# Optimization experiments

Measured on AMD Instinct MI355X. Metric: run time of the kernel, lower is better.

## Reference

```python
import jax, jax.numpy as jnp
import numpy as np

HIDDEN = 1024
RANK = 4
INPUT = 16
ALPHA = 0.1
BASE_SCALE = 500.0
B = 32
T = 1024


def setup_inputs() -> dict:
    key = jax.random.key(0)
    k1, k2, k3, k4 = jax.random.split(key, 4)
    std = HIDDEN ** -0.25  # matches cov ~ I/sqrt(hidden) in original init
    x = jax.random.normal(k1, (B, T, INPUT), dtype=jnp.float32)
    m = jax.random.normal(k2, (HIDDEN, RANK), dtype=jnp.float32) * std
    n = jax.random.normal(k3, (HIDDEN, RANK), dtype=jnp.float32) * std
    I_mat = jax.random.normal(k4, (HIDDEN, INPUT), dtype=jnp.float32) * std
    return {"x": x, "m": m, "n": n, "I_mat": I_mat}


def reference(x, m, n, I_mat):
    # J = (m @ n.T) * base_scale / hidden ; recurrent term (J @ tanh(h).T).T
    # == tanh(h) @ J.T == ((tanh(h) @ n) @ m.T) * scale  (low-rank form, same math)
    scale = BASE_SCALE / HIDDEN

    def step(h, x_t):
        rec = (jnp.tanh(h) @ n) @ m.T * scale          # [B, H]
        dh = -h + rec + x_t @ I_mat.T                  # [B, H]
        h = h + ALPHA * dh
        return h, h

    h0 = jnp.zeros((x.shape[0], HIDDEN), dtype=x.dtype)
    _, hiddens = jax.lax.scan(step, h0, jnp.swapaxes(x, 0, 1))  # [T, B, H]
    hiddens = jnp.swapaxes(hiddens, 0, 1)                       # [B, T, H]

    span = jnp.concatenate([m, I_mat], axis=1)   # [H, RANK+INPUT]
    proj = jnp.linalg.pinv(span)                 # [RANK+INPUT, H]
    # (pinv(span) @ hiddens.permute(0,2,1)).permute(0,2,1)
    return jnp.einsum('ph,bth->btp', proj, hiddens)  # [B, T, RANK+INPUT]
```

## Files before the change

kernel.cpp:

```cpp
#include <hip/hip_runtime.h>
#include <math.h>

#define HIDDEN_ 1024
#define RANK_ 4
#define INPUT_ 16
#define T_ 1024
#define BATCH_ 32

#define NTHREADS_ 256
#define NWAVES_ (NTHREADS_ / 64)
#define EPT_ (HIDDEN_ / NTHREADS_)

__device__ __forceinline__ float fast_exp2(float x) {
#if defined(__has_builtin)
#if __has_builtin(__builtin_amdgcn_exp2f)
    return __builtin_amdgcn_exp2f(x);
#else
    return exp2f(x);
#endif
#else
    return exp2f(x);
#endif
}

__device__ __forceinline__ float fast_rcp(float x) {
#if defined(__has_builtin)
#if __has_builtin(__builtin_amdgcn_rcpf)
    return __builtin_amdgcn_rcpf(x);
#else
    return 1.0f / x;
#endif
#else
    return 1.0f / x;
#endif
}

__device__ __forceinline__ float tanh_fast(float x) {
    float e = fast_exp2(x * 2.885390081777926815f);
    return fmaf(-2.0f, fast_rcp(e + 1.0f), 1.0f);
}

#define DPP_ADD(v, ctrl)                                                          \
    do {                                                                          \
        int _t = __builtin_amdgcn_update_dpp(0, __float_as_int(v), (ctrl), 0xf,   \
                                             0xf, true);                          \
        (v) += __int_as_float(_t);                                                \
    } while (0)

#define WAVE_RED_TO_LANE63(v)  \
    DPP_ADD(v, 0x111);         \
    DPP_ADD(v, 0x112);         \
    DPP_ADD(v, 0x114);         \
    DPP_ADD(v, 0x118);         \
    DPP_ADD(v, 0x142);         \
    DPP_ADD(v, 0x143)

__global__ __launch_bounds__(NTHREADS_) void rnn_scan_kernel(
    const float* __restrict__ x,
    const float* __restrict__ m,
    const float* __restrict__ n,
    const float* __restrict__ imat,
    float* __restrict__ out)
{
    const int b    = blockIdx.x;
    const int tid  = threadIdx.x;
    const int wave = tid >> 6;
    const int lane = tid & 63;

    const float kd   = 0.9f;
    const float krec = 0.1f * (500.0f / 1024.0f);
    const float kin  = 0.1f;

    float h[EPT_];
    float mrs[EPT_][RANK_];
    float nr[EPT_][RANK_];
    float Irs[EPT_][INPUT_];

#pragma unroll
    for (int j = 0; j < EPT_; ++j) {
        const int hidx = tid * EPT_ + j;
        h[j] = 0.0f;
        const float4 mv = *(const float4*)(m + hidx * RANK_);
        mrs[j][0] = krec * mv.x; mrs[j][1] = krec * mv.y;
        mrs[j][2] = krec * mv.z; mrs[j][3] = krec * mv.w;
        const float4 nv = *(const float4*)(n + hidx * RANK_);
        nr[j][0] = nv.x; nr[j][1] = nv.y; nr[j][2] = nv.z; nr[j][3] = nv.w;
#pragma unroll
        for (int q = 0; q < 4; ++q) {
            const float4 iv = *(const float4*)(imat + hidx * INPUT_ + q * 4);
            Irs[j][q*4+0] = kin * iv.x; Irs[j][q*4+1] = kin * iv.y;
            Irs[j][q*4+2] = kin * iv.z; Irs[j][q*4+3] = kin * iv.w;
        }
    }

    __shared__ float4 part[2][NWAVES_];

    const float* xb = x + (size_t)b * T_ * INPUT_;
    float* ob = out + (size_t)b * T_ * (RANK_ + INPUT_);

    float y = 0.0f;
    const bool is_xy = (tid >= 4 && tid < 20);
    float xy = is_xy ? xb[tid - 4] : 0.0f;

    for (int t = 0; t < T_; ++t) {
        const float* xt = xb + t * INPUT_;
        float xr[INPUT_];
#pragma unroll
        for (int q = 0; q < 4; ++q) {
            float4 v = ((const float4*)xt)[q];
            xr[q*4+0] = v.x; xr[q*4+1] = v.y; xr[q*4+2] = v.z; xr[q*4+3] = v.w;
        }
        float xy_nxt = 0.0f;
        if (is_xy) {
            int tn = (t + 1 < T_) ? (t + 1) : t;
            xy_nxt = xb[tn * INPUT_ + (tid - 4)];
        }

        float th[EPT_];
#pragma unroll
        for (int j = 0; j < EPT_; ++j) th[j] = tanh_fast(h[j]);

        float p0 = th[0] * nr[0][0], p1 = th[0] * nr[0][1];
        float p2 = th[0] * nr[0][2], p3 = th[0] * nr[0][3];
#pragma unroll
        for (int j = 1; j < EPT_; ++j) {
            p0 = fmaf(th[j], nr[j][0], p0);
            p1 = fmaf(th[j], nr[j][1], p1);
            p2 = fmaf(th[j], nr[j][2], p2);
            p3 = fmaf(th[j], nr[j][3], p3);
        }

        DPP_ADD(p0, 0x111); DPP_ADD(p1, 0x111); DPP_ADD(p2, 0x111); DPP_ADD(p3, 0x111);
        DPP_ADD(p0, 0x112); DPP_ADD(p1, 0x112); DPP_ADD(p2, 0x112); DPP_ADD(p3, 0x112);
        DPP_ADD(p0, 0x114); DPP_ADD(p1, 0x114); DPP_ADD(p2, 0x114); DPP_ADD(p3, 0x114);
        DPP_ADD(p0, 0x118); DPP_ADD(p1, 0x118); DPP_ADD(p2, 0x118); DPP_ADD(p3, 0x118);
        DPP_ADD(p0, 0x142); DPP_ADD(p1, 0x142); DPP_ADD(p2, 0x142); DPP_ADD(p3, 0x142);
        DPP_ADD(p0, 0x143); DPP_ADD(p1, 0x143); DPP_ADD(p2, 0x143); DPP_ADD(p3, 0x143);

        if (lane == 63) part[t & 1][wave] = make_float4(p0, p1, p2, p3);
        __syncthreads();

        const float4 q0 = part[t & 1][0];
        const float4 q1 = part[t & 1][1];
        const float4 q2 = part[t & 1][2];
        const float4 q3 = part[t & 1][3];
        const float s0 = (q0.x + q1.x) + (q2.x + q3.x);
        const float s1 = (q0.y + q1.y) + (q2.y + q3.y);
        const float s2 = (q0.z + q1.z) + (q2.z + q3.z);
        const float s3 = (q0.w + q1.w) + (q2.w + q3.w);

#pragma unroll
        for (int j = 0; j < EPT_; ++j) {
            float a = xr[0] * Irs[j][0];
#pragma unroll
            for (int i = 1; i < INPUT_; ++i)
                a = fmaf(xr[i], Irs[j][i], a);
            a = fmaf(s0, mrs[j][0], a);
            a = fmaf(s1, mrs[j][1], a);
            a = fmaf(s2, mrs[j][2], a);
            a = fmaf(s3, mrs[j][3], a);
            h[j] = fmaf(kd, h[j], a);
        }

        if (tid < 20) {
            float drive;
            if (tid < 4) {
                float sv = (tid == 0) ? s0 : (tid == 1) ? s1 : (tid == 2) ? s2 : s3;
                drive = krec * sv;
            } else {
                drive = kin * xy;
            }
            y = fmaf(kd, y, drive);
            ob[t * 20 + tid] = y;
        }
        xy = xy_nxt;
    }
}

extern "C" void kernel_launch(void* const* d_in, const int* in_sizes, int n_in,
                              void* d_out, int out_size, void* d_ws, size_t ws_size,
                              hipStream_t stream) {
    const float* x    = (const float*)d_in[0];
    const float* m    = (const float*)d_in[1];
    const float* n    = (const float*)d_in[2];
    const float* imat = (const float*)d_in[3];
    float* out = (float*)d_out;

    rnn_scan_kernel<<<dim3(BATCH_), dim3(NTHREADS_), 0, stream>>>(x, m, n, imat, out);
}
```

Baseline: 607.0 us.

## Prefetch next-step inputs, split input FMA chain, replace syncthreads with raw barrier

Loads x for step t+1 inside the loop body and carries it in registers, so global load latency overlaps the current step's work. The input-projection dot product now runs before the reduced recurrent sums are read and uses two accumulators to shorten the dependency chain. __syncthreads is replaced with an explicit lgkmcnt wait plus s_barrier, a vzero register keeps the x loads as vector loads, and asm constraints pin the weights in VGPRs. Also sets launch_bounds min blocks to 1 and unrolls the loop by 2, which may raise register pressure.

After: 658.5 us. 8.5% more time.

```diff
diff --git a/kernel.cpp b/kernel.cpp
--- a/kernel.cpp
+++ b/kernel.cpp
@@ -47,15 +47,7 @@
         (v) += __int_as_float(_t);                                                \
     } while (0)
 
-#define WAVE_RED_TO_LANE63(v)  \
-    DPP_ADD(v, 0x111);         \
-    DPP_ADD(v, 0x112);         \
-    DPP_ADD(v, 0x114);         \
-    DPP_ADD(v, 0x118);         \
-    DPP_ADD(v, 0x142);         \
-    DPP_ADD(v, 0x143)
-
-__global__ __launch_bounds__(NTHREADS_) void rnn_scan_kernel(
+__global__ __launch_bounds__(NTHREADS_, 1) void rnn_scan_kernel(
     const float* __restrict__ x,
     const float* __restrict__ m,
     const float* __restrict__ n,
@@ -93,29 +85,41 @@
         }
     }
 
+#pragma unroll
+    for (int j = 0; j < EPT_; ++j) {
+#pragma unroll
+        for (int i = 0; i < INPUT_; ++i) asm volatile("" : "+v"(Irs[j][i]));
+#pragma unroll
+        for (int r = 0; r < RANK_; ++r) {
+            asm volatile("" : "+v"(mrs[j][r]));
+            asm volatile("" : "+v"(nr[j][r]));
+        }
+    }
+
     __shared__ float4 part[2][NWAVES_];
+
+    int vzero;
+    asm volatile("v_mov_b32 %0, 0" : "=v"(vzero));
 
     const float* xb = x + (size_t)b * T_ * INPUT_;
     float* ob = out + (size_t)b * T_ * (RANK_ + INPUT_);
 
     float y = 0.0f;
     const bool is_xy = (tid >= 4 && tid < 20);
-    float xy = is_xy ? xb[tid - 4] : 0.0f;
-
+    float xy = is_xy ? xb[vzero + (tid - 4)] : 0.0f;
+
+    float xr[INPUT_];
+    {
+        const float4* xp = (const float4*)xb;
+#pragma unroll
+        for (int q = 0; q < 4; ++q) {
+            float4 v = xp[vzero + q];
+            xr[q*4+0] = v.x; xr[q*4+1] = v.y; xr[q*4+2] = v.z; xr[q*4+3] = v.w;
+        }
+    }
+
+#pragma unroll 2
     for (int t = 0; t < T_; ++t) {
-        const float* xt = xb + t * INPUT_;
-        float xr[INPUT_];
-#pragma unroll
-        for (int q = 0; q < 4; ++q) {
-            float4 v = ((const float4*)xt)[q];
-            xr[q*4+0] = v.x; xr[q*4+1] = v.y; xr[q*4+2] = v.z; xr[q*4+3] = v.w;
-        }
-        float xy_nxt = 0.0f;
-        if (is_xy) {
-            int tn = (t + 1 < T_) ? (t + 1) : t;
-            xy_nxt = xb[tn * INPUT_ + (tid - 4)];
-        }
-
         float th[EPT_];
 #pragma unroll
         for (int j = 0; j < EPT_; ++j) th[j] = tanh_fast(h[j]);
@@ -138,12 +142,36 @@
         DPP_ADD(p0, 0x143); DPP_ADD(p1, 0x143); DPP_ADD(p2, 0x143); DPP_ADD(p3, 0x143);
 
         if (lane == 63) part[t & 1][wave] = make_float4(p0, p1, p2, p3);
-        __syncthreads();
+
+        asm volatile("s_waitcnt lgkmcnt(0)\n\ts_barrier" ::: "memory");
 
         const float4 q0 = part[t & 1][0];
         const float4 q1 = part[t & 1][1];
         const float4 q2 = part[t & 1][2];
         const float4 q3 = part[t & 1][3];
+
+        const int tn = (t + 1 < T_) ? (t + 1) : t;
+        const float4* xp = (const float4*)(xb + tn * INPUT_);
+        float4 xv0 = xp[vzero + 0];
+        float4 xv1 = xp[vzero + 1];
+        float4 xv2 = xp[vzero + 2];
+        float4 xv3 = xp[vzero + 3];
+        float xy_nxt = 0.0f;
+        if (is_xy) xy_nxt = xb[tn * INPUT_ + vzero + (tid - 4)];
+
+        float ax[EPT_];
+#pragma unroll
+        for (int j = 0; j < EPT_; ++j) {
+            float a = xr[0] * Irs[j][0];
+            float c = xr[1] * Irs[j][1];
+#pragma unroll
+            for (int i = 2; i < INPUT_; i += 2) {
+                a = fmaf(xr[i],     Irs[j][i],     a);
+                c = fmaf(xr[i + 1], Irs[j][i + 1], c);
+            }
+            ax[j] = a + c;
+        }
+
         const float s0 = (q0.x + q1.x) + (q2.x + q3.x);
         const float s1 = (q0.y + q1.y) + (q2.y + q3.y);
         const float s2 = (q0.z + q1.z) + (q2.z + q3.z);
@@ -151,11 +179,7 @@
 
 #pragma unroll
         for (int j = 0; j < EPT_; ++j) {
-            float a = xr[0] * Irs[j][0];
-#pragma unroll
-            for (int i = 1; i < INPUT_; ++i)
-                a = fmaf(xr[i], Irs[j][i], a);
-            a = fmaf(s0, mrs[j][0], a);
+            float a = fmaf(s0, mrs[j][0], ax[j]);
             a = fmaf(s1, mrs[j][1], a);
             a = fmaf(s2, mrs[j][2], a);
             a = fmaf(s3, mrs[j][3], a);
@@ -173,6 +197,11 @@
             y = fmaf(kd, y, drive);
             ob[t * 20 + tid] = y;
         }
+
+        xr[0]  = xv0.x; xr[1]  = xv0.y; xr[2]  = xv0.z; xr[3]  = xv0.w;
+        xr[4]  = xv1.x; xr[5]  = xv1.y; xr[6]  = xv1.z; xr[7]  = xv1.w;
+        xr[8]  = xv2.x; xr[9]  = xv2.y; xr[10] = xv2.z; xr[11] = xv2.w;
+        xr[12] = xv3.x; xr[13] = xv3.y; xr[14] = xv3.z; xr[15] = xv3.w;
         xy = xy_nxt;
     }
 }
```

## Split block into scan and helper waves that precompute input drive via LDS

Applied to the files above, without the earlier changes.

Doubles the block to 512 threads. Half run the recurrent scan. The other half precompute the x_t @ I^T drive one step ahead into a 4-deep LDS ring, stage x in 64-step chunks into shared memory, and write the outputs. This takes the 16-term input dot product and the global x loads off the serial critical path of each timestep. The cost is more threads taking part in each per-step barrier, a raw s_barrier in inline asm, and more LDS traffic.

New measurement: 518.7 us, median of 2. 1.17x faster.

```diff
diff --git a/kernel.cpp b/kernel.cpp
--- a/kernel.cpp
+++ b/kernel.cpp
@@ -7,9 +7,11 @@
 #define T_ 1024
 #define BATCH_ 32
 
-#define NTHREADS_ 256
-#define NWAVES_ (NTHREADS_ / 64)
-#define EPT_ (HIDDEN_ / NTHREADS_)
+#define NT_ 512
+#define SCANT_ 256
+#define EPT_ 4
+#define CH_ 64
+#define NCH_ (T_ / CH_)
 
 __device__ __forceinline__ float fast_exp2(float x) {
 #if defined(__has_builtin)
@@ -47,133 +49,182 @@
         (v) += __int_as_float(_t);                                                \
     } while (0)
 
-#define WAVE_RED_TO_LANE63(v)  \
-    DPP_ADD(v, 0x111);         \
-    DPP_ADD(v, 0x112);         \
-    DPP_ADD(v, 0x114);         \
-    DPP_ADD(v, 0x118);         \
-    DPP_ADD(v, 0x142);         \
-    DPP_ADD(v, 0x143)
-
-__global__ __launch_bounds__(NTHREADS_) void rnn_scan_kernel(
+__global__ __launch_bounds__(NT_)
+__attribute__((amdgpu_waves_per_eu(2, 2)))
+void rnn_fused_kernel(
     const float* __restrict__ x,
     const float* __restrict__ m,
     const float* __restrict__ n,
     const float* __restrict__ imat,
     float* __restrict__ out)
 {
+    const int tid  = threadIdx.x;
+    const int lane = tid & 63;
     const int b    = blockIdx.x;
-    const int tid  = threadIdx.x;
-    const int wave = tid >> 6;
-    const int lane = tid & 63;
+    const bool is_scan = (tid < SCANT_);
 
     const float kd   = 0.9f;
     const float krec = 0.1f * (500.0f / 1024.0f);
     const float kin  = 0.1f;
+
+    __shared__ float4 part[2][SCANT_ / 64];
+    __shared__ float  axs[4][HIDDEN_];
+    __shared__ float  xs[2][CH_ * INPUT_];
+
+    const float* xb = x + (size_t)b * T_ * INPUT_;
+    float* ob = out + (size_t)b * T_ * (RANK_ + INPUT_);
 
     float h[EPT_];
     float mrs[EPT_][RANK_];
     float nr[EPT_][RANK_];
     float Irs[EPT_][INPUT_];
-
-#pragma unroll
-    for (int j = 0; j < EPT_; ++j) {
-        const int hidx = tid * EPT_ + j;
-        h[j] = 0.0f;
-        const float4 mv = *(const float4*)(m + hidx * RANK_);
-        mrs[j][0] = krec * mv.x; mrs[j][1] = krec * mv.y;
-        mrs[j][2] = krec * mv.z; mrs[j][3] = krec * mv.w;
-        const float4 nv = *(const float4*)(n + hidx * RANK_);
-        nr[j][0] = nv.x; nr[j][1] = nv.y; nr[j][2] = nv.z; nr[j][3] = nv.w;
+    float4 xstage = make_float4(0.f, 0.f, 0.f, 0.f);
+    float y = 0.0f;
+    int yoff = 0;
+
+    if (is_scan) {
+#pragma unroll
+        for (int j = 0; j < EPT_; ++j) {
+            const int hidx = tid * EPT_ + j;
+            h[j] = 0.0f;
+            const float4 mv = *(const float4*)(m + hidx * RANK_);
+            mrs[j][0] = krec * mv.x; mrs[j][1] = krec * mv.y;
+            mrs[j][2] = krec * mv.z; mrs[j][3] = krec * mv.w;
+            const float4 nv = *(const float4*)(n + hidx * RANK_);
+            nr[j][0] = nv.x; nr[j][1] = nv.y; nr[j][2] = nv.z; nr[j][3] = nv.w;
+        }
+    } else {
+        const int tH = tid - SCANT_;
+        yoff = (tH >= 4 && tH < 20) ? (tH - 4) : 0;
+#pragma unroll
+        for (int j = 0; j < EPT_; ++j) {
+            const int hidx = tH * EPT_ + j;
+#pragma unroll
+            for (int q = 0; q < 4; ++q) {
+                const float4 iv = *(const float4*)(imat + hidx * INPUT_ + q * 4);
+                Irs[j][q*4+0] = kin * iv.x; Irs[j][q*4+1] = kin * iv.y;
+                Irs[j][q*4+2] = kin * iv.z; Irs[j][q*4+3] = kin * iv.w;
+            }
+        }
+        float4 c0 = *(const float4*)(xb + tH * 4);
+        *(float4*)&xs[0][tH * 4] = c0;
+        xstage = *(const float4*)(xb + CH_ * INPUT_ + tH * 4);
+        float xv[INPUT_];
 #pragma unroll
         for (int q = 0; q < 4; ++q) {
-            const float4 iv = *(const float4*)(imat + hidx * INPUT_ + q * 4);
-            Irs[j][q*4+0] = kin * iv.x; Irs[j][q*4+1] = kin * iv.y;
-            Irs[j][q*4+2] = kin * iv.z; Irs[j][q*4+3] = kin * iv.w;
-        }
+            const float4 v = ((const float4*)xb)[q];
+            xv[q*4+0] = v.x; xv[q*4+1] = v.y; xv[q*4+2] = v.z; xv[q*4+3] = v.w;
+        }
+        float av[EPT_];
+#pragma unroll
+        for (int j = 0; j < EPT_; ++j) {
+            float a = xv[0] * Irs[j][0];
+            float c = xv[1] * Irs[j][1];
+#pragma unroll
+            for (int i = 2; i < INPUT_; i += 2) {
+                a = fmaf(xv[i],     Irs[j][i],     a);
+                c = fmaf(xv[i + 1], Irs[j][i + 1], c);
+            }
+            av[j] = a + c;
+        }
+        *(float4*)&axs[0][tH * 4] = make_float4(av[0], av[1], av[2], av[3]);
     }
-
-    __shared__ float4 part[2][NWAVES_];
-
-    const float* xb = x + (size_t)b * T_ * INPUT_;
-    float* ob = out + (size_t)b * T_ * (RANK_ + INPUT_);
-
-    float y = 0.0f;
-    const bool is_xy = (tid >= 4 && tid < 20);
-    float xy = is_xy ? xb[tid - 4] : 0.0f;
+    __syncthreads();
 
     for (int t = 0; t < T_; ++t) {
-        const float* xt = xb + t * INPUT_;
-        float xr[INPUT_];
-#pragma unroll
-        for (int q = 0; q < 4; ++q) {
-            float4 v = ((const float4*)xt)[q];
-            xr[q*4+0] = v.x; xr[q*4+1] = v.y; xr[q*4+2] = v.z; xr[q*4+3] = v.w;
-        }
-        float xy_nxt = 0.0f;
-        if (is_xy) {
-            int tn = (t + 1 < T_) ? (t + 1) : t;
-            xy_nxt = xb[tn * INPUT_ + (tid - 4)];
-        }
-
-        float th[EPT_];
-#pragma unroll
-        for (int j = 0; j < EPT_; ++j) th[j] = tanh_fast(h[j]);
-
-        float p0 = th[0] * nr[0][0], p1 = th[0] * nr[0][1];
-        float p2 = th[0] * nr[0][2], p3 = th[0] * nr[0][3];
-#pragma unroll
-        for (int j = 1; j < EPT_; ++j) {
-            p0 = fmaf(th[j], nr[j][0], p0);
-            p1 = fmaf(th[j], nr[j][1], p1);
-            p2 = fmaf(th[j], nr[j][2], p2);
-            p3 = fmaf(th[j], nr[j][3], p3);
-        }
-
-        DPP_ADD(p0, 0x111); DPP_ADD(p1, 0x111); DPP_ADD(p2, 0x111); DPP_ADD(p3, 0x111);
-        DPP_ADD(p0, 0x112); DPP_ADD(p1, 0x112); DPP_ADD(p2, 0x112); DPP_ADD(p3, 0x112);
-        DPP_ADD(p0, 0x114); DPP_ADD(p1, 0x114); DPP_ADD(p2, 0x114); DPP_ADD(p3, 0x114);
-        DPP_ADD(p0, 0x118); DPP_ADD(p1, 0x118); DPP_ADD(p2, 0x118); DPP_ADD(p3, 0x118);
-        DPP_ADD(p0, 0x142); DPP_ADD(p1, 0x142); DPP_ADD(p2, 0x142); DPP_ADD(p3, 0x142);
-        DPP_ADD(p0, 0x143); DPP_ADD(p1, 0x143); DPP_ADD(p2, 0x143); DPP_ADD(p3, 0x143);
-
-        if (lane == 63) part[t & 1][wave] = make_float4(p0, p1, p2, p3);
-        __syncthreads();
-
-        const float4 q0 = part[t & 1][0];
-        const float4 q1 = part[t & 1][1];
-        const float4 q2 = part[t & 1][2];
-        const float4 q3 = part[t & 1][3];
-        const float s0 = (q0.x + q1.x) + (q2.x + q3.x);
-        const float s1 = (q0.y + q1.y) + (q2.y + q3.y);
-        const float s2 = (q0.z + q1.z) + (q2.z + q3.z);
-        const float s3 = (q0.w + q1.w) + (q2.w + q3.w);
-
-#pragma unroll
-        for (int j = 0; j < EPT_; ++j) {
-            float a = xr[0] * Irs[j][0];
-#pragma unroll
-            for (int i = 1; i < INPUT_; ++i)
-                a = fmaf(xr[i], Irs[j][i], a);
-            a = fmaf(s0, mrs[j][0], a);
-            a = fmaf(s1, mrs[j][1], a);
-            a = fmaf(s2, mrs[j][2], a);
-            a = fmaf(s3, mrs[j][3], a);
-            h[j] = fmaf(kd, h[j], a);
-        }
-
-        if (tid < 20) {
-            float drive;
-            if (tid < 4) {
-                float sv = (tid == 0) ? s0 : (tid == 1) ? s1 : (tid == 2) ? s2 : s3;
-                drive = krec * sv;
-            } else {
-                drive = kin * xy;
-            }
-            y = fmaf(kd, y, drive);
-            ob[t * 20 + tid] = y;
-        }
-        xy = xy_nxt;
+        if (is_scan) {
+            float th[EPT_];
+#pragma unroll
+            for (int j = 0; j < EPT_; ++j) th[j] = tanh_fast(h[j]);
+
+            float p0 = th[0] * nr[0][0], p1 = th[0] * nr[0][1];
+            float p2 = th[0] * nr[0][2], p3 = th[0] * nr[0][3];
+#pragma unroll
+            for (int j = 1; j < EPT_; ++j) {
+                p0 = fmaf(th[j], nr[j][0], p0);
+                p1 = fmaf(th[j], nr[j][1], p1);
+                p2 = fmaf(th[j], nr[j][2], p2);
+                p3 = fmaf(th[j], nr[j][3], p3);
+            }
+
+            DPP_ADD(p0, 0x111); DPP_ADD(p1, 0x111); DPP_ADD(p2, 0x111); DPP_ADD(p3, 0x111);
+            DPP_ADD(p0, 0x112); DPP_ADD(p1, 0x112); DPP_ADD(p2, 0x112); DPP_ADD(p3, 0x112);
+            DPP_ADD(p0, 0x114); DPP_ADD(p1, 0x114); DPP_ADD(p2, 0x114); DPP_ADD(p3, 0x114);
+            DPP_ADD(p0, 0x118); DPP_ADD(p1, 0x118); DPP_ADD(p2, 0x118); DPP_ADD(p3, 0x118);
+            DPP_ADD(p0, 0x142); DPP_ADD(p1, 0x142); DPP_ADD(p2, 0x142); DPP_ADD(p3, 0x142);
+            DPP_ADD(p0, 0x143); DPP_ADD(p1, 0x143); DPP_ADD(p2, 0x143); DPP_ADD(p3, 0x143);
+
+            if (lane == 63) part[t & 1][tid >> 6] = make_float4(p0, p1, p2, p3);
+        } else {
+            const int tH = tid - SCANT_;
+            const int tn = (t + 1 < T_) ? (t + 1) : (T_ - 1);
+            const float* xsp = &xs[(tn >> 6) & 1][(tn & 63) * INPUT_];
+            const float4 xa  = ((const float4*)xsp)[0];
+            const float4 xb4 = ((const float4*)xsp)[1];
+            const float4 xc  = ((const float4*)xsp)[2];
+            const float4 xd  = ((const float4*)xsp)[3];
+            float av[EPT_];
+#pragma unroll
+            for (int j = 0; j < EPT_; ++j) {
+                float a = xa.x * Irs[j][0];
+                float c = xa.y * Irs[j][1];
+                a = fmaf(xa.z,  Irs[j][2],  a);  c = fmaf(xa.w,  Irs[j][3],  c);
+                a = fmaf(xb4.x, Irs[j][4],  a);  c = fmaf(xb4.y, Irs[j][5],  c);
+                a = fmaf(xb4.z, Irs[j][6],  a);  c = fmaf(xb4.w, Irs[j][7],  c);
+                a = fmaf(xc.x,  Irs[j][8],  a);  c = fmaf(xc.y,  Irs[j][9],  c);
+                a = fmaf(xc.z,  Irs[j][10], a);  c = fmaf(xc.w,  Irs[j][11], c);
+                a = fmaf(xd.x,  Irs[j][12], a);  c = fmaf(xd.y,  Irs[j][13], c);
+                a = fmaf(xd.z,  Irs[j][14], a);  c = fmaf(xd.w,  Irs[j][15], c);
+                av[j] = a + c;
+            }
+            *(float4*)&axs[(t + 1) & 3][tH * 4] =
+                make_float4(av[0], av[1], av[2], av[3]);
+        }
+
+        asm volatile("s_waitcnt lgkmcnt(0)\n\ts_barrier" ::: "memory");
+
+        if (is_scan) {
+            const float4 q0 = part[t & 1][0];
+            const float4 q1 = part[t & 1][1];
+            const float4 q2 = part[t & 1][2];
+            const float4 q3 = part[t & 1][3];
+            const float4 axv = *(const float4*)&axs[t & 3][tid * 4];
+
+            const float4 sv = (q0 + q1) + (q2 + q3);
+            const float s0 = sv.x, s1 = sv.y, s2 = sv.z, s3 = sv.w;
+            const float aq[EPT_] = {axv.x, axv.y, axv.z, axv.w};
+#pragma unroll
+            for (int j = 0; j < EPT_; ++j) {
+                float a01 = fmaf(s1, mrs[j][1], fmaf(s0, mrs[j][0], aq[j]));
+                float a23 = fmaf(s3, mrs[j][3], s2 * mrs[j][2]);
+                h[j] = fmaf(kd, h[j], a01 + a23);
+            }
+        } else {
+            const int tH = tid - SCANT_;
+            if ((t & (CH_ - 1)) == 0) {
+                const int c = t >> 6;
+                *(float4*)&xs[(c + 1) & 1][tH * 4] = xstage;
+                const int cl = (c + 2 < NCH_) ? (c + 2) : (NCH_ - 1);
+                xstage = *(const float4*)(xb + cl * CH_ * INPUT_ + tH * 4);
+            }
+            if (tH < 20) {
+                const float4 q0 = part[t & 1][0];
+                const float4 q1 = part[t & 1][1];
+                const float4 q2 = part[t & 1][2];
+                const float4 q3 = part[t & 1][3];
+                const float4 sv = (q0 + q1) + (q2 + q3);
+                float drive;
+                if (tH < 4) {
+                    const float svv = (tH == 0) ? sv.x : (tH == 1) ? sv.y
+                                    : (tH == 2) ? sv.z : sv.w;
+                    drive = krec * svv;
+                } else {
+                    drive = kin * xs[(t >> 6) & 1][(t & 63) * INPUT_ + yoff];
+                }
+                y = fmaf(kd, y, drive);
+                ob[t * 20 + tH] = y;
+            }
+        }
     }
 }
 
@@ -186,5 +237,5 @@
     const float* imat = (const float*)d_in[3];
     float* out = (float*)d_out;
 
-    rnn_scan_kernel<<<dim3(BATCH_), dim3(NTHREADS_), 0, stream>>>(x, m, n, imat, out);
-}
+    rnn_fused_kernel<<<dim3(BATCH_), dim3(NT_), 0, stream>>>(x, m, n, imat, out);
+}
```
